# Optimization experiments

Measured on AMD Instinct MI355X. Metric: run time of the kernel, lower is better.

Reference implementation:

```python
import jax, jax.numpy as jnp
import numpy as np

EMBED_DIM = 1024
CONTEXT_LEN = 2048
NUM_HEADS = 16
HEAD_DIM = EMBED_DIM // NUM_HEADS
BATCH = 2
SEQ = 2048


def setup_inputs() -> dict:
    key = jax.random.key(0)
    ks = jax.random.split(key, 6)
    s = 1.0 / np.sqrt(EMBED_DIM)
    x = jax.random.normal(ks[0], (BATCH, SEQ, EMBED_DIM), dtype=jnp.float32)
    # nn.Linear weights stored as [out, in]; we keep [in, out] for x @ W
    W_q = jax.random.uniform(ks[1], (EMBED_DIM, EMBED_DIM), jnp.float32, -s, s)
    W_k = jax.random.uniform(ks[2], (EMBED_DIM, EMBED_DIM), jnp.float32, -s, s)
    W_v = jax.random.uniform(ks[3], (EMBED_DIM, EMBED_DIM), jnp.float32, -s, s)
    W_o = jax.random.uniform(ks[4], (EMBED_DIM, EMBED_DIM), jnp.float32, -s, s)
    b_o = jax.random.uniform(ks[5], (EMBED_DIM,), jnp.float32, -s, s)
    return {"x": x, "W_q": W_q, "W_k": W_k, "W_v": W_v, "W_o": W_o, "b_o": b_o}


def reference(x, W_q, W_k, W_v, W_o, b_o):
    b, s, _ = x.shape
    # project and split heads: [b, s, e] -> [b, h, s, d]
    def heads(t):
        return t.reshape(b, s, NUM_HEADS, HEAD_DIM).transpose(0, 2, 1, 3)
    q = heads(x @ W_q)
    k = heads(x @ W_k)
    v = heads(x @ W_v)
    scores = jnp.einsum("bhqd,bhkd->bhqk", q, k)  # full seq x seq scores
    causal = jnp.triu(jnp.ones((s, s), dtype=bool), k=1)
    scores = jnp.where(causal, -jnp.inf, scores)
    attn = jax.nn.softmax(scores / np.sqrt(HEAD_DIM).astype(np.float32), axis=-1)
    ctx = jnp.einsum("bhqk,bhkd->bhqd", attn, v)
    ctx = ctx.transpose(0, 2, 1, 3).reshape(b, s, EMBED_DIM)
    return ctx @ W_o + b_o
```

## Files before the change

kernel.cpp:

```cpp
#include <hip/hip_runtime.h>

#define EMBED 1024
#define SEQL  2048
#define NHEAD 16
#define HDIM  64
#define NBATCH 2
#define MROWS 4096

typedef __attribute__((ext_vector_type(4))) float  f32x4;
typedef __attribute__((ext_vector_type(8))) __bf16 bf16x8;

__device__ __forceinline__ short f2bf(float f){
  __bf16 h = (__bf16)f;
  union { __bf16 h; short s; } u; u.h = h;
  return u.s;
}

#define GLDS(gp, lp) __builtin_amdgcn_global_load_lds( \
    (const __attribute__((address_space(1))) void*)(gp), \
    (__attribute__((address_space(3))) void*)(lp), 16, 0, 0)

#define WAITV(N) do { asm volatile("s_waitcnt vmcnt(" #N ")" ::: "memory"); \
                      __builtin_amdgcn_sched_barrier(0); } while(0)
#define BARRIER() do { __builtin_amdgcn_s_barrier(); \
                       __builtin_amdgcn_sched_barrier(0); } while(0)

__global__ __launch_bounds__(256) void prep_kernel(const float* __restrict__ x,
    const float* __restrict__ W0, const float* __restrict__ W1,
    const float* __restrict__ W2, const float* __restrict__ W3,
    short* __restrict__ Xb, short* __restrict__ WtAll){
  const int z = blockIdx.z;
  if (z < 4){
    __shared__ float T[64][65];
    const int idx = blockIdx.y*32 + blockIdx.x;
    if (idx >= 256) return;
    const float* W = (z==0)?W0:(z==1)?W1:(z==2)?W2:W3;
    short* Wt = WtAll + z*(EMBED*EMBED);
    const int bx = (idx & 15)*64;
    const int by = (idx >> 4)*64;
    const int c4 = (threadIdx.x & 15)*4;
    const int tr = threadIdx.x >> 4;
    #pragma unroll
    for (int i=0;i<4;++i){
      int r = 16*i + tr;
      float4 v = *(const float4*)(W + (by + r)*EMBED + bx + c4);
      T[c4+0][r] = v.x; T[c4+1][r] = v.y; T[c4+2][r] = v.z; T[c4+3][r] = v.w;
    }
    __syncthreads();
    #pragma unroll
    for (int i=0;i<4;++i){
      int n = 16*i + tr;
      short4 o;
      o.x = f2bf(T[n][c4+0]); o.y = f2bf(T[n][c4+1]);
      o.z = f2bf(T[n][c4+2]); o.w = f2bf(T[n][c4+3]);
      *(short4*)(Wt + (bx + n)*EMBED + by + c4) = o;
    }
  } else {
    const int blk = (z-4)*1024 + blockIdx.y*32 + blockIdx.x;
    const int i = (blk*256 + threadIdx.x)*4;
    float4 v = *(const float4*)(x + i);
    short4 o; o.x=f2bf(v.x); o.y=f2bf(v.y); o.z=f2bf(v.z); o.w=f2bf(v.w);
    *(short4*)(Xb + i) = o;
  }
}

__device__ __forceinline__ void gemm_tile_128(const short* __restrict__ A,
    const short* __restrict__ Bt, short* As, short* Bs, int m0, int n0, f32x4 acc[4][4]){
  const int tid  = threadIdx.x;
  const int lane = tid & 63;
  const int wid  = tid >> 6;
  const int wrow = (wid >> 1) * 64, wcol = (wid & 1) * 64;
  const int arow = tid >> 2, acol8 = (tid & 3) * 8;
  const int l15 = lane & 15, lg = lane >> 4;

  auto STAGE = [&](int b, int k0){
    short* as = As + b*4096;
    short* bs = Bs + b*4096;
    GLDS(A  + (m0      + arow) * 1024 + k0 + acol8, as + tid*8);
    GLDS(A  + (m0 + 64 + arow) * 1024 + k0 + acol8, as + 2048 + tid*8);
    GLDS(Bt + (n0      + arow) * 1024 + k0 + acol8, bs + tid*8);
    GLDS(Bt + (n0 + 64 + arow) * 1024 + k0 + acol8, bs + 2048 + tid*8);
  };

  STAGE(0, 0); STAGE(1, 32);
  WAITV(4);
  BARRIER();
  for (int k = 0; k < 32; ++k){
    if (k + 2 < 32) STAGE((k+2)%3, (k+2)*32);
    const short* as = As + (k%3)*4096;
    const short* bs = Bs + (k%3)*4096;
    bf16x8 a[4], b[4];
    #pragma unroll
    for (int i=0;i<4;++i) a[i] = *(const bf16x8*)(as + (wrow+16*i+l15)*32 + 8*lg);
    #pragma unroll
    for (int j=0;j<4;++j) b[j] = *(const bf16x8*)(bs + (wcol+16*j+l15)*32 + 8*lg);
    #pragma unroll
    for (int i=0;i<4;++i)
      #pragma unroll
      for (int j=0;j<4;++j)
        acc[i][j] = __builtin_amdgcn_mfma_f32_16x16x32_bf16(a[i], b[j], acc[i][j], 0,0,0);
    if (k + 2 < 32) { WAITV(4); } else { WAITV(0); }
    BARRIER();
  }
}

__device__ __forceinline__ void gemm_tile_64(const short* __restrict__ A,
    const short* __restrict__ Bt, short* As, short* Bs, int m0, int n0, f32x4 acc[2][4]){
  const int tid  = threadIdx.x;
  const int lane = tid & 63;
  const int wid  = tid >> 6;
  const int wrow = (wid >> 1) * 32, wcol = (wid & 1) * 64;
  const int arow = tid >> 2, acol8 = (tid & 3) * 8;
  const int l15 = lane & 15, lg = lane >> 4;

  auto STAGE = [&](int b, int k0){
    short* as = As + b*2048;
    short* bs = Bs + b*4096;
    GLDS(A  + (m0      + arow) * 1024 + k0 + acol8, as + tid*8);
    GLDS(Bt + (n0      + arow) * 1024 + k0 + acol8, bs + tid*8);
    GLDS(Bt + (n0 + 64 + arow) * 1024 + k0 + acol8, bs + 2048 + tid*8);
  };

  STAGE(0, 0); STAGE(1, 32);
  WAITV(3);
  BARRIER();
  for (int k = 0; k < 32; ++k){
    if (k + 2 < 32) STAGE((k+2)%3, (k+2)*32);
    const short* as = As + (k%3)*2048;
    const short* bs = Bs + (k%3)*4096;
    bf16x8 a[2], b[4];
    #pragma unroll
    for (int i=0;i<2;++i) a[i] = *(const bf16x8*)(as + (wrow+16*i+l15)*32 + 8*lg);
    #pragma unroll
    for (int j=0;j<4;++j) b[j] = *(const bf16x8*)(bs + (wcol+16*j+l15)*32 + 8*lg);
    #pragma unroll
    for (int i=0;i<2;++i)
      #pragma unroll
      for (int j=0;j<4;++j)
        acc[i][j] = __builtin_amdgcn_mfma_f32_16x16x32_bf16(a[i], b[j], acc[i][j], 0,0,0);
    if (k + 2 < 32) { WAITV(3); } else { WAITV(0); }
    BARRIER();
  }
}

__global__ __launch_bounds__(256) void gemm_qkv_kernel(const short* __restrict__ Xb,
    const short* __restrict__ WtAll, short* __restrict__ Q, short* __restrict__ K,
    short* __restrict__ Vt){
  __shared__ __align__(16) short SH[24576];
  short* As = SH;
  short* Bs = SH + 12288;
  const int m0 = blockIdx.x*128, n0 = blockIdx.y*128, z = blockIdx.z;
  const short* Bt = WtAll + z*(EMBED*EMBED);
  f32x4 acc[4][4] = {};
  gemm_tile_128(Xb, Bt, As, Bs, m0, n0, acc);
  const int tid  = threadIdx.x;
  const int lane = tid & 63;
  const int wid  = tid >> 6;
  const int wrow = (wid >> 1) * 64, wcol = (wid & 1) * 64;
  const int l15 = lane & 15, lg = lane >> 4;
  const int bb = m0 >> 11, srow0 = m0 & 2047;

  if (z < 2){
    short* out = z ? K : Q;
    const float qscl = (z==0) ? (0.125f * 1.44269504f) : 1.0f;
    #pragma unroll
    for (int i=0;i<4;++i)
      #pragma unroll
      for (int j=0;j<4;++j)
        #pragma unroll
        for (int r=0;r<4;++r){
          int m = m0 + wrow + 16*i + 4*lg + r;
          int n = n0 + wcol + 16*j + l15;
          int srow = m & 2047, hh = n >> 6, d = n & 63;
          out[(((bb<<4)+hh)*SEQL + srow)*HDIM + d] = f2bf(acc[i][j][r] * qscl);
        }
  } else {
    short* T = SH;
    #pragma unroll
    for (int i=0;i<4;++i)
      #pragma unroll
      for (int j=0;j<4;++j){
        int n_loc = wcol + 16*j + l15;
        int mb    = wrow + 16*i + 4*lg;
        short4 pk;
        pk.x = f2bf(acc[i][j][0]); pk.y = f2bf(acc[i][j][1]);
        pk.z = f2bf(acc[i][j][2]); pk.w = f2bf(acc[i][j][3]);
        *(short4*)(T + n_loc*128 + (mb ^ ((n_loc & 7) << 3))) = pk;
      }
    __syncthreads();
    #pragma unroll
    for (int it=0; it<8; ++it){
      int n_loc = 16*it + (tid >> 4);
      int mch   = (tid & 15) * 8;
      int4 v = *(const int4*)(T + n_loc*128 + (mch ^ ((n_loc & 7) << 3)));
      int n_glob = n0 + n_loc;
      int hh = n_glob >> 6, d = n_glob & 63;
      *(int4*)(Vt + (((bb<<4)+hh)*HDIM + d)*SEQL + srow0 + mch) = v;
    }
  }
}

__global__ __launch_bounds__(256) void gemm_out_kernel(const short* __restrict__ Ctx,
    const short* __restrict__ WtO, const float* __restrict__ bias, float* __restrict__ out){
  __shared__ __align__(16) short As[3*2048], Bs[3*4096];
  const int m0 = blockIdx.x*64, n0 = blockIdx.y*128;
  f32x4 acc[2][4] = {};
  gemm_tile_64(Ctx, WtO, As, Bs, m0, n0, acc);
  const int lane = threadIdx.x & 63;
  const int wid  = threadIdx.x >> 6;
  const int wrow = (wid >> 1) * 32, wcol = (wid & 1) * 64;
  const int l15 = lane & 15, lg = lane >> 4;
  #pragma unroll
  for (int i=0;i<2;++i)
    #pragma unroll
    for (int j=0;j<4;++j)
      #pragma unroll
      for (int r=0;r<4;++r){
        int m = m0 + wrow + 16*i + 4*lg + r;
        int n = n0 + wcol + 16*j + l15;
        out[m*EMBED + n] = acc[i][j][r] + bias[n];
      }
}

__global__ __launch_bounds__(512, 4) void attn_kernel(const short* __restrict__ Q,
    const short* __restrict__ K, const short* __restrict__ Vt, short* __restrict__ Ctx){
  __shared__ __align__(16) char lds[49152];
  const int tid  = threadIdx.x;
  const int lane = tid & 63;
  const int wid  = tid >> 6;
  const int bid   = blockIdx.x;
  const int xcd   = bid & 7;
  const int i7    = bid >> 3;
  const int bh    = xcd + 8*(i7 & 3);
  const int cidx  = i7 >> 2;
  const int chunk = (cidx < 8) ? cidx : 23 - cidx;
  const int q0blk = chunk * 128;
  const int ntblk = 2*chunk + 2;
  const int q0w   = q0blk + 16*wid;
  const int qlast = q0w + 15;

  const short* Qh  = Q  + bh*(SEQL*HDIM);
  const char*  KhB = (const char*)(K  + bh*(SEQL*HDIM));
  const char*  VhB = (const char*)(Vt + bh*(HDIM*SEQL));
  const int l15 = lane & 15, lg = lane >> 4;
  const int lg20 = 20 * lg;
  const int swE = (l15 & 7) << 3;
  const int swB = (l15 & 7) << 4;
  const int laneRow = lane >> 3;
  const int colSwz  = 16 * ((lane & 7) ^ laneRow);
  const int r0 = 8 * wid;

  const short* qp = Qh + (q0w + l15)*HDIM + 8*lg;
  bf16x8 bq0 = *(const bf16x8*)qp;
  bf16x8 bq1 = *(const bf16x8*)(qp + 32);

  f32x4 acc[4];
  #pragma unroll
  for (int j=0; j<4; ++j) acc[j] = (f32x4){0.f,0.f,0.f,0.f};
  float mrun = -3e30f, lrun = 0.f;

  short* pw = (short*)(lds + 32768 + wid*2048);

  auto STAGE = [&](int b, int t){
    char* kb = lds + b*16384;
    char* vb = kb + 8192;
    const int kv0 = t*64;
    GLDS(KhB + (kv0 + r0 + laneRow)*128 + colSwz, kb + r0*128);
    GLDS(VhB + (r0 + laneRow)*4096 + kv0*2 + colSwz, vb + r0*128);
  };

  STAGE(0, 0);
  __syncthreads();

  int cur = 0;
  for (int t = 0; t < ntblk; ++t){
    const int kv0 = t*64;
    if (t + 1 < ntblk) STAGE(cur ^ 1, t + 1);
    if (kv0 <= qlast){
      const char* kb = lds + cur*16384;
      const char* vb = kb + 8192;
      f32x4 sc[4];
      __builtin_amdgcn_s_setprio(1);
      #pragma unroll
      for (int c=0; c<4; ++c){
        const char* kr = kb + (16*c + l15)*128;
        bf16x8 k0 = *(const bf16x8*)(kr + ((16*lg) ^ swB));
        bf16x8 k1 = *(const bf16x8*)(kr + ((64 + 16*lg) ^ swB));
        f32x4 z = (f32x4){0.f,0.f,0.f,0.f};
        z = __builtin_amdgcn_mfma_f32_16x16x32_bf16(k0, bq0, z, 0,0,0);
        z = __builtin_amdgcn_mfma_f32_16x16x32_bf16(k1, bq1, z, 0,0,0);
        sc[c] = z;
      }
      __builtin_amdgcn_s_setprio(0);
      if (kv0 + 63 > q0w){
        #pragma unroll
        for (int c=0; c<4; ++c)
          #pragma unroll
          for (int r=0; r<4; ++r)
            if (kv0 + 16*c + 4*lg + r > q0w + l15) sc[c][r] = -3e30f;
      }
      float cm[4];
      #pragma unroll
      for (int c=0; c<4; ++c)
        cm[c] = fmaxf(fmaxf(sc[c][0], sc[c][1]), fmaxf(sc[c][2], sc[c][3]));
      float pm = fmaxf(fmaxf(cm[0], cm[1]), fmaxf(cm[2], cm[3]));
      pm = fmaxf(pm, __shfl_xor(pm, 16));
      pm = fmaxf(pm, __shfl_xor(pm, 32));
      const int resc = !__all(pm <= mrun);
      float mn = mrun, ss = 1.0f;
      if (resc){
        mn = fmaxf(mrun, pm);
        ss = __builtin_amdgcn_exp2f(mrun - mn);
        mrun = mn;
      }
      #pragma unroll
      for (int c=0; c<4; ++c)
        #pragma unroll
        for (int r=0; r<4; ++r)
          sc[c][r] = __builtin_amdgcn_exp2f(sc[c][r] - mn);
      float cs[4];
      #pragma unroll
      for (int c=0; c<4; ++c)
        cs[c] = (sc[c][0] + sc[c][1]) + (sc[c][2] + sc[c][3]);
      float ls = (cs[0] + cs[1]) + (cs[2] + cs[3]);
      ls += __shfl_xor(ls, 16);
      ls += __shfl_xor(ls, 32);
      if (resc){
        lrun = lrun*ss + ls;
        float srg[4];
        #pragma unroll
        for (int r=0; r<4; ++r) srg[r] = __shfl(ss, lg20 + r);
        #pragma unroll
        for (int j=0; j<4; ++j)
          #pragma unroll
          for (int r=0; r<4; ++r) acc[j][r] *= srg[r];
      } else {
        lrun += ls;
      }
      #pragma unroll
      for (int c=0; c<4; ++c){
        short4 pk;
        pk.x = f2bf(sc[c][0]); pk.y = f2bf(sc[c][1]);
        pk.z = f2bf(sc[c][2]); pk.w = f2bf(sc[c][3]);
        *(short4*)(pw + l15*64 + ((16*c + 4*lg) ^ swE)) = pk;
      }
      bf16x8 pa0 = *(const bf16x8*)(pw + l15*64 + ((8*lg)      ^ swE));
      bf16x8 pa1 = *(const bf16x8*)(pw + l15*64 + ((32 + 8*lg) ^ swE));
      __builtin_amdgcn_s_setprio(1);
      #pragma unroll
      for (int j=0; j<4; ++j){
        const char* vrp = vb + (16*j + l15)*128;
        bf16x8 v0 = *(const bf16x8*)(vrp + ((16*lg) ^ swB));
        bf16x8 v1 = *(const bf16x8*)(vrp + ((64 + 16*lg) ^ swB));
        acc[j] = __builtin_amdgcn_mfma_f32_16x16x32_bf16(pa0, v0, acc[j], 0,0,0);
        acc[j] = __builtin_amdgcn_mfma_f32_16x16x32_bf16(pa1, v1, acc[j], 0,0,0);
      }
      __builtin_amdgcn_s_setprio(0);
    }
    __syncthreads();
    cur ^= 1;
  }

  const int bb = bh >> 4, hh = bh & 15;
  float lr[4];
  #pragma unroll
  for (int r=0; r<4; ++r) lr[r] = __builtin_amdgcn_rcpf(__shfl(lrun, lg20 + r));
  #pragma unroll
  for (int j=0; j<4; ++j)
    #pragma unroll
    for (int r=0; r<4; ++r){
      int qg = q0w + 4*lg + r;
      Ctx[(bb*SEQL + qg)*EMBED + hh*HDIM + 16*j + l15] = f2bf(acc[j][r] * lr[r]);
    }
}

extern "C" void kernel_launch(void* const* d_in, const int* in_sizes, int n_in,
                              void* d_out, int out_size, void* d_ws, size_t ws_size,
                              hipStream_t stream){
  const float* x  = (const float*)d_in[0];
  const float* Wq = (const float*)d_in[1];
  const float* Wk = (const float*)d_in[2];
  const float* Wv = (const float*)d_in[3];
  const float* Wo = (const float*)d_in[4];
  const float* bo = (const float*)d_in[5];
  float* out = (float*)d_out;

  char* ws = (char*)d_ws;
  const size_t MB = 1u << 20;
  short* Xb  = (short*)(ws +  0*MB);
  short* Wt  = (short*)(ws +  8*MB);
  short* Q   = (short*)(ws + 16*MB);
  short* Kk  = (short*)(ws + 24*MB);
  short* Vt  = (short*)(ws + 32*MB);
  short* Ctx = (short*)(ws + 40*MB);

  prep_kernel<<<dim3(32,32,8), 256, 0, stream>>>(x, Wq, Wk, Wv, Wo, Xb, Wt);
  gemm_qkv_kernel<<<dim3(32,8,3), 256, 0, stream>>>(Xb, Wt, Q, Kk, Vt);
  attn_kernel<<<512, 512, 0, stream>>>(Q, Kk, Vt, Ctx);
  gemm_out_kernel<<<dim3(64,8), 256, 0, stream>>>(Ctx, Wt + 3*(EMBED*EMBED), bo, out);
}
```

Before: 107.5 us.

## Process two KV tiles per attention iteration with quad-buffered LDS staging

The attention loop now handles two 64-key tiles per iteration, computing both score blocks, one combined max/sum reduction and rescale, then two PV MFMA passes. LDS grows to four K/V stage buffers so two tiles are prefetched ahead. This is meant to halve barriers and online-softmax reductions per key. In exchange it raises LDS use, which can lower blocks per CU, and adds register pressure from the two score sets.

```diff
diff --git a/kernel.cpp b/kernel.cpp
--- a/kernel.cpp
+++ b/kernel.cpp
@@ -224,7 +224,7 @@
 
 __global__ __launch_bounds__(512, 4) void attn_kernel(const short* __restrict__ Q,
     const short* __restrict__ K, const short* __restrict__ Vt, short* __restrict__ Ctx){
-  __shared__ __align__(16) char lds[49152];
+  __shared__ __align__(16) char lds[81920];
   const int tid  = threadIdx.x;
   const int lane = tid & 63;
   const int wid  = tid >> 6;
@@ -235,7 +235,7 @@
   const int cidx  = i7 >> 2;
   const int chunk = (cidx < 8) ? cidx : 23 - cidx;
   const int q0blk = chunk * 128;
-  const int ntblk = 2*chunk + 2;
+  const int ntp   = chunk + 1;
   const int q0w   = q0blk + 16*wid;
   const int qlast = q0w + 15;
 
@@ -259,7 +259,7 @@
   for (int j=0; j<4; ++j) acc[j] = (f32x4){0.f,0.f,0.f,0.f};
   float mrun = -3e30f, lrun = 0.f;
 
-  short* pw = (short*)(lds + 32768 + wid*2048);
+  short* pw = (short*)(lds + 65536 + wid*2048);
 
   auto STAGE = [&](int b, int t){
     char* kb = lds + b*16384;
@@ -269,41 +269,62 @@
     GLDS(VhB + (r0 + laneRow)*4096 + kv0*2 + colSwz, vb + r0*128);
   };
 
-  STAGE(0, 0);
+  auto QKHALF = [&](const char* kb, f32x4 sc[4]){
+    #pragma unroll
+    for (int c=0; c<4; ++c){
+      const char* kr = kb + (16*c + l15)*128;
+      bf16x8 k0 = *(const bf16x8*)(kr + ((16*lg) ^ swB));
+      bf16x8 k1 = *(const bf16x8*)(kr + ((64 + 16*lg) ^ swB));
+      f32x4 z = (f32x4){0.f,0.f,0.f,0.f};
+      z = __builtin_amdgcn_mfma_f32_16x16x32_bf16(k0, bq0, z, 0,0,0);
+      z = __builtin_amdgcn_mfma_f32_16x16x32_bf16(k1, bq1, z, 0,0,0);
+      sc[c] = z;
+    }
+  };
+
+  STAGE(0, 0); STAGE(1, 1);
   __syncthreads();
 
-  int cur = 0;
-  for (int t = 0; t < ntblk; ++t){
-    const int kv0 = t*64;
-    if (t + 1 < ntblk) STAGE(cur ^ 1, t + 1);
-    if (kv0 <= qlast){
-      const char* kb = lds + cur*16384;
-      const char* vb = kb + 8192;
-      f32x4 sc[4];
+  for (int tp = 0; tp < ntp; ++tp){
+    const int t0   = 2*tp;
+    const int kv00 = t0*64;
+    const int kv01 = kv00 + 64;
+    if (tp + 1 < ntp){ STAGE((t0+2)&3, t0+2); STAGE((t0+3)&3, t0+3); }
+    if (kv00 <= qlast){
+      const char* kb0 = lds + (t0&3)*16384;
+      const char* kb1 = lds + ((t0+1)&3)*16384;
+      const bool  h1  = (kv01 <= qlast);
+      f32x4 sc0[4], sc1[4];
       __builtin_amdgcn_s_setprio(1);
-      #pragma unroll
-      for (int c=0; c<4; ++c){
-        const char* kr = kb + (16*c + l15)*128;
-        bf16x8 k0 = *(const bf16x8*)(kr + ((16*lg) ^ swB));
-        bf16x8 k1 = *(const bf16x8*)(kr + ((64 + 16*lg) ^ swB));
-        f32x4 z = (f32x4){0.f,0.f,0.f,0.f};
-        z = __builtin_amdgcn_mfma_f32_16x16x32_bf16(k0, bq0, z, 0,0,0);
-        z = __builtin_amdgcn_mfma_f32_16x16x32_bf16(k1, bq1, z, 0,0,0);
-        sc[c] = z;
-      }
+      QKHALF(kb0, sc0);
+      if (h1) QKHALF(kb1, sc1);
       __builtin_amdgcn_s_setprio(0);
-      if (kv0 + 63 > q0w){
+      if (kv00 + 63 > q0w){
         #pragma unroll
         for (int c=0; c<4; ++c)
           #pragma unroll
           for (int r=0; r<4; ++r)
-            if (kv0 + 16*c + 4*lg + r > q0w + l15) sc[c][r] = -3e30f;
+            if (kv00 + 16*c + 4*lg + r > q0w + l15) sc0[c][r] = -3e30f;
+      }
+      if (h1 && kv01 + 63 > q0w){
+        #pragma unroll
+        for (int c=0; c<4; ++c)
+          #pragma unroll
+          for (int r=0; r<4; ++r)
+            if (kv01 + 16*c + 4*lg + r > q0w + l15) sc1[c][r] = -3e30f;
       }
       float cm[4];
       #pragma unroll
       for (int c=0; c<4; ++c)
-        cm[c] = fmaxf(fmaxf(sc[c][0], sc[c][1]), fmaxf(sc[c][2], sc[c][3]));
+        cm[c] = fmaxf(fmaxf(sc0[c][0], sc0[c][1]), fmaxf(sc0[c][2], sc0[c][3]));
       float pm = fmaxf(fmaxf(cm[0], cm[1]), fmaxf(cm[2], cm[3]));
+      if (h1){
+        float dm[4];
+        #pragma unroll
+        for (int c=0; c<4; ++c)
+          dm[c] = fmaxf(fmaxf(sc1[c][0], sc1[c][1]), fmaxf(sc1[c][2], sc1[c][3]));
+        pm = fmaxf(pm, fmaxf(fmaxf(dm[0], dm[1]), fmaxf(dm[2], dm[3])));
+      }
       pm = fmaxf(pm, __shfl_xor(pm, 16));
       pm = fmaxf(pm, __shfl_xor(pm, 32));
       const int resc = !__all(pm <= mrun);
@@ -317,12 +338,24 @@
       for (int c=0; c<4; ++c)
         #pragma unroll
         for (int r=0; r<4; ++r)
-          sc[c][r] = __builtin_amdgcn_exp2f(sc[c][r] - mn);
+          sc0[c][r] = __builtin_amdgcn_exp2f(sc0[c][r] - mn);
       float cs[4];
       #pragma unroll
       for (int c=0; c<4; ++c)
-        cs[c] = (sc[c][0] + sc[c][1]) + (sc[c][2] + sc[c][3]);
+        cs[c] = (sc0[c][0] + sc0[c][1]) + (sc0[c][2] + sc0[c][3]);
       float ls = (cs[0] + cs[1]) + (cs[2] + cs[3]);
+      if (h1){
+        #pragma unroll
+        for (int c=0; c<4; ++c)
+          #pragma unroll
+          for (int r=0; r<4; ++r)
+            sc1[c][r] = __builtin_amdgcn_exp2f(sc1[c][r] - mn);
+        float ds[4];
+        #pragma unroll
+        for (int c=0; c<4; ++c)
+          ds[c] = (sc1[c][0] + sc1[c][1]) + (sc1[c][2] + sc1[c][3]);
+        ls += (ds[0] + ds[1]) + (ds[2] + ds[3]);
+      }
       ls += __shfl_xor(ls, 16);
       ls += __shfl_xor(ls, 32);
       if (resc){
@@ -340,25 +373,49 @@
       #pragma unroll
       for (int c=0; c<4; ++c){
         short4 pk;
-        pk.x = f2bf(sc[c][0]); pk.y = f2bf(sc[c][1]);
-        pk.z = f2bf(sc[c][2]); pk.w = f2bf(sc[c][3]);
+        pk.x = f2bf(sc0[c][0]); pk.y = f2bf(sc0[c][1]);
+        pk.z = f2bf(sc0[c][2]); pk.w = f2bf(sc0[c][3]);
         *(short4*)(pw + l15*64 + ((16*c + 4*lg) ^ swE)) = pk;
       }
-      bf16x8 pa0 = *(const bf16x8*)(pw + l15*64 + ((8*lg)      ^ swE));
-      bf16x8 pa1 = *(const bf16x8*)(pw + l15*64 + ((32 + 8*lg) ^ swE));
-      __builtin_amdgcn_s_setprio(1);
-      #pragma unroll
-      for (int j=0; j<4; ++j){
-        const char* vrp = vb + (16*j + l15)*128;
-        bf16x8 v0 = *(const bf16x8*)(vrp + ((16*lg) ^ swB));
-        bf16x8 v1 = *(const bf16x8*)(vrp + ((64 + 16*lg) ^ swB));
-        acc[j] = __builtin_amdgcn_mfma_f32_16x16x32_bf16(pa0, v0, acc[j], 0,0,0);
-        acc[j] = __builtin_amdgcn_mfma_f32_16x16x32_bf16(pa1, v1, acc[j], 0,0,0);
-      }
-      __builtin_amdgcn_s_setprio(0);
+      {
+        bf16x8 pa0 = *(const bf16x8*)(pw + l15*64 + ((8*lg)      ^ swE));
+        bf16x8 pa1 = *(const bf16x8*)(pw + l15*64 + ((32 + 8*lg) ^ swE));
+        const char* vb = kb0 + 8192;
+        __builtin_amdgcn_s_setprio(1);
+        #pragma unroll
+        for (int j=0; j<4; ++j){
+          const char* vrp = vb + (16*j + l15)*128;
+          bf16x8 v0 = *(const bf16x8*)(vrp + ((16*lg) ^ swB));
+          bf16x8 v1 = *(const bf16x8*)(vrp + ((64 + 16*lg) ^ swB));
+          acc[j] = __builtin_amdgcn_mfma_f32_16x16x32_bf16(pa0, v0, acc[j], 0,0,0);
+          acc[j] = __builtin_amdgcn_mfma_f32_16x16x32_bf16(pa1, v1, acc[j], 0,0,0);
+        }
+        __builtin_amdgcn_s_setprio(0);
+      }
+      if (h1){
+        #pragma unroll
+        for (int c=0; c<4; ++c){
+          short4 pk;
+          pk.x = f2bf(sc1[c][0]); pk.y = f2bf(sc1[c][1]);
+          pk.z = f2bf(sc1[c][2]); pk.w = f2bf(sc1[c][3]);
+          *(short4*)(pw + l15*64 + ((16*c + 4*lg) ^ swE)) = pk;
+        }
+        bf16x8 pa0 = *(const bf16x8*)(pw + l15*64 + ((8*lg)      ^ swE));
+        bf16x8 pa1 = *(const bf16x8*)(pw + l15*64 + ((32 + 8*lg) ^ swE));
+        const char* vb = kb1 + 8192;
+        __builtin_amdgcn_s_setprio(1);
+        #pragma unroll
+        for (int j=0; j<4; ++j){
+          const char* vrp = vb + (16*j + l15)*128;
+          bf16x8 v0 = *(const bf16x8*)(vrp + ((16*lg) ^ swB));
+          bf16x8 v1 = *(const bf16x8*)(vrp + ((64 + 16*lg) ^ swB));
+          acc[j] = __builtin_amdgcn_mfma_f32_16x16x32_bf16(pa0, v0, acc[j], 0,0,0);
+          acc[j] = __builtin_amdgcn_mfma_f32_16x16x32_bf16(pa1, v1, acc[j], 0,0,0);
+        }
+        __builtin_amdgcn_s_setprio(0);
+      }
     }
     __syncthreads();
-    cur ^= 1;
   }
 
   const int bb = bh >> 4, hh = bh & 15;
```

Result: faster. 102.7 us (-4.5%).
